# Kernel optimization log

Hardware: AMD Instinct MI355X
Metric: run time of the kernel (lower is better)

Reference implementation:

```python
import jax, jax.numpy as jnp
import numpy as np

CHUNK = 128      # chunk_size
NUM_BITS = 6     # log2(num_experts=64)


def setup_inputs() -> dict:
    key = jax.random.key(0)
    k1, k2, k3 = jax.random.split(key, 3)
    B, L, D, E = 4, 4096, 1024, 64
    x = jax.random.normal(k1, (B, L, D), dtype=jnp.float32)
    expert_weights = jax.random.normal(k2, (E, D, D), dtype=jnp.float32) * 0.02
    hyperplanes = jax.random.normal(k3, (D, NUM_BITS), dtype=jnp.float32)
    return {"x": x, "expert_weights": expert_weights, "hyperplanes": hyperplanes}


def reference(x, expert_weights, hyperplanes):
    # x: [B, L, D]; L divisible by CHUNK (no padding path taken)
    B, L, D = x.shape
    C = L // CHUNK
    xr = x.reshape(B, C, CHUNK, D)

    # --- LSH (SimHash) router, chunk-level ---
    chunk_emb = xr.mean(axis=2)                      # [B, C, D]
    proj = chunk_emb @ hyperplanes                   # [B, C, bits]
    bits = (proj > 0).astype(jnp.int32)
    powers = (2 ** jnp.arange(NUM_BITS)).astype(jnp.int32)
    e1 = jnp.sum(bits * powers, axis=-1)             # [B, C]
    weakest = jnp.argmin(jnp.abs(proj), axis=-1)     # weakest hyperplane bit
    flip = (2 ** weakest).astype(jnp.int32)
    e2 = jnp.bitwise_xor(e1, flip)                   # second expert: flip weakest bit
    # gates are all 1.0 and router_threshold=0.0 -> confidence_mask = 1.0

    # --- per-chunk expert weight gather + bmm combine (top-2 average) ---
    out = jnp.zeros_like(xr)
    for idx in (e1, e2):
        w = expert_weights[idx]                      # [B, C, D, D] gathered
        out = out + jnp.einsum('bcld,bcde->bcle', xr, w)
    out = out * 0.5
    # dropout p=0.0 / eval -> identity
    return out.reshape(B, L, D)
```

## Files before the change

kernel.cpp:

```cpp
#include <hip/hip_runtime.h>
#include <hip/hip_bf16.h>


#define BD 4
#define LD 4096
#define DD 1024
#define ED 64
#define CHUNKD 128
#define NBITS 6
#define NCHUNK 128

typedef __bf16 bf16_8 __attribute__((ext_vector_type(8)));
typedef __bf16 bf16_4 __attribute__((ext_vector_type(4)));
typedef float floatx4 __attribute__((ext_vector_type(4)));

__global__ __launch_bounds__(256) void sum_cvt_kernel(
    const float* __restrict__ x, __bf16* __restrict__ a, double* __restrict__ csum)
{
    const int chunk = blockIdx.x >> 3;
    const int tg = blockIdx.x & 7;
    const size_t base = (size_t)chunk * CHUNKD * DD + (size_t)tg * 16 * DD;
    const float* xc = x + base;
    __bf16* ac = a + base;
    const int t = threadIdx.x;

    double s0 = 0, s1 = 0, s2 = 0, s3 = 0;
    #pragma unroll 4
    for (int tok = 0; tok < 16; ++tok) {
        const float4 v = *(const float4*)(xc + tok * DD + t * 4);
        bf16_4 o;
        o[0] = (__bf16)v.x; o[1] = (__bf16)v.y; o[2] = (__bf16)v.z; o[3] = (__bf16)v.w;
        *(bf16_4*)(ac + tok * DD + t * 4) = o;
        s0 += (double)v.x; s1 += (double)v.y; s2 += (double)v.z; s3 += (double)v.w;
    }
    double* c = csum + (size_t)chunk * DD + t * 4;
    atomicAdd(c + 0, s0); atomicAdd(c + 1, s1);
    atomicAdd(c + 2, s2); atomicAdd(c + 3, s3);
}

__global__ __launch_bounds__(256) void router2_kernel(
    const double* __restrict__ csum, const float* __restrict__ hyp,
    int* __restrict__ eidx)
{
    const int chunk = blockIdx.x;
    const int t = threadIdx.x;
    double pj[NBITS];
    #pragma unroll
    for (int j = 0; j < NBITS; ++j) pj[j] = 0.0;
    #pragma unroll
    for (int i = 0; i < 4; ++i) {
        const int d = t + i * 256;
        const double emb = csum[(size_t)chunk * DD + d] * (1.0 / 128.0);
        #pragma unroll
        for (int j = 0; j < NBITS; ++j)
            pj[j] += emb * (double)hyp[d * NBITS + j];
    }
    #pragma unroll
    for (int off = 32; off > 0; off >>= 1) {
        #pragma unroll
        for (int j = 0; j < NBITS; ++j)
            pj[j] += __shfl_down(pj[j], off, 64);
    }
    __shared__ double red[4][NBITS];
    const int wave = t >> 6, lane = t & 63;
    if (lane == 0) {
        #pragma unroll
        for (int j = 0; j < NBITS; ++j) red[wave][j] = pj[j];
    }
    __syncthreads();
    if (t == 0) {
        int e1 = 0, weakest = 0;
        double best = 1e300;
        #pragma unroll
        for (int j = 0; j < NBITS; ++j) {
            double p = red[0][j] + red[1][j] + red[2][j] + red[3][j];
            if (p > 0.0) e1 |= (1 << j);
            double aa = fabs(p);
            if (aa < best) { best = aa; weakest = j; }
        }
        eidx[chunk * 2 + 0] = e1;
        eidx[chunk * 2 + 1] = e1 ^ (1 << weakest);
    }
}

__global__ __launch_bounds__(256) void wcvt_kernel(
    const float* __restrict__ W, __bf16* __restrict__ Wt)
{
    const int e = blockIdx.x >> 4;
    const int n0 = (blockIdx.x & 15) * 64;
    const float* We = W + (size_t)e * DD * DD;
    __bf16* Wte = Wt + (size_t)e * DD * DD;
    const int nl = threadIdx.x & 63;
    const int kc = threadIdx.x >> 6;
    const int n = n0 + nl;

    for (int it = 0; it < 32; ++it) {
        const int k = it * 32 + kc * 8;
        float v[8];
        #pragma unroll
        for (int j = 0; j < 8; ++j) v[j] = We[(size_t)(k + j) * DD + n];
        bf16_8 o;
        #pragma unroll
        for (int j = 0; j < 8; ++j) o[j] = (__bf16)v[j];
        *(bf16_8*)(&Wte[(size_t)n * DD + k]) = o;
    }
}

__global__ __launch_bounds__(256) void ffn_gemm_bf16(
    const __bf16* __restrict__ Abf,
    const __bf16* __restrict__ Wt,
    const int* __restrict__ eidx,
    float* __restrict__ out)
{
    __shared__ __bf16 Als[128 * 32];
    __shared__ __bf16 Bls[128 * 32];

    const int bx = blockIdx.x;
    const int chunk = bx >> 3;
    const int n0 = (bx & 7) * 128;
    const int t = threadIdx.x;
    const int lane = t & 63;
    const int wave = t >> 6;
    const int wm = wave >> 1;
    const int wn = wave & 1;
    const int lr = lane & 15;
    const int q  = lane >> 4;

    const int ee[2] = {eidx[chunk * 2 + 0], eidx[chunk * 2 + 1]};

    const __bf16* Ag = Abf + (size_t)chunk * CHUNKD * DD;

    floatx4 acc[4][4] = {};

    for (int xp = 0; xp < 2; ++xp) {
        const __bf16* Bg = Wt + (size_t)ee[xp] * (DD * DD) + (size_t)n0 * DD;
        for (int k0 = 0; k0 < DD; k0 += 32) {
            #pragma unroll
            for (int i = 0; i < 2; ++i) {
                const int rb = wave * 2 + i;
                const __bf16* ga = Ag + (size_t)(rb * 16 + lr) * DD + k0 + q * 8;
                __builtin_amdgcn_global_load_lds(
                    (const __attribute__((address_space(1))) void*)ga,
                    (__attribute__((address_space(3))) void*)(&Als[rb * 512]),
                    16, 0, 0);
            }
            #pragma unroll
            for (int i = 0; i < 2; ++i) {
                const int rb = wave * 2 + i;
                const __bf16* gb = Bg + (size_t)(rb * 16 + lr) * DD + k0 + q * 8;
                __builtin_amdgcn_global_load_lds(
                    (const __attribute__((address_space(1))) void*)gb,
                    (__attribute__((address_space(3))) void*)(&Bls[rb * 512]),
                    16, 0, 0);
            }
            __syncthreads();

            bf16_8 af[4], bfr[4];
            #pragma unroll
            for (int mt = 0; mt < 4; ++mt)
                af[mt] = *(const bf16_8*)(&Als[(wm * 4 + mt) * 512 + lane * 8]);
            #pragma unroll
            for (int nt = 0; nt < 4; ++nt)
                bfr[nt] = *(const bf16_8*)(&Bls[(wn * 4 + nt) * 512 + lane * 8]);
            #pragma unroll
            for (int mt = 0; mt < 4; ++mt) {
                #pragma unroll
                for (int nt = 0; nt < 4; ++nt)
                    acc[mt][nt] = __builtin_amdgcn_mfma_f32_16x16x32_bf16(
                        af[mt], bfr[nt], acc[mt][nt], 0, 0, 0);
            }
            __syncthreads();
        }
    }

    const size_t orow0 = (size_t)chunk * CHUNKD;
    #pragma unroll
    for (int mt = 0; mt < 4; ++mt) {
        #pragma unroll
        for (int nt = 0; nt < 4; ++nt) {
            const int col = n0 + wn * 64 + nt * 16 + lr;
            #pragma unroll
            for (int r = 0; r < 4; ++r) {
                const int row = wm * 64 + mt * 16 + q * 4 + r;
                out[(orow0 + row) * DD + col] = acc[mt][nt][r] * 0.5f;
            }
        }
    }
}

__global__ __launch_bounds__(256) void router_kernel(
    const float* __restrict__ x, const float* __restrict__ hyp,
    int* __restrict__ eidx)
{
    const int chunk = blockIdx.x;
    const int t = threadIdx.x;
    const float* xc = x + (size_t)chunk * CHUNKD * DD;
    double cs[4] = {0.0, 0.0, 0.0, 0.0};
    for (int tok = 0; tok < CHUNKD; ++tok) {
        const float* row = xc + tok * DD;
        #pragma unroll
        for (int i = 0; i < 4; ++i) cs[i] += (double)row[t + i * 256];
    }
    double pj[NBITS];
    #pragma unroll
    for (int j = 0; j < NBITS; ++j) pj[j] = 0.0;
    #pragma unroll
    for (int i = 0; i < 4; ++i) {
        const int d = t + i * 256;
        const double emb = cs[i] * (1.0 / 128.0);
        #pragma unroll
        for (int j = 0; j < NBITS; ++j) pj[j] += emb * (double)hyp[d * NBITS + j];
    }
    #pragma unroll
    for (int off = 32; off > 0; off >>= 1) {
        #pragma unroll
        for (int j = 0; j < NBITS; ++j) pj[j] += __shfl_down(pj[j], off, 64);
    }
    __shared__ double red[4][NBITS];
    const int wave = t >> 6, lane = t & 63;
    if (lane == 0) {
        #pragma unroll
        for (int j = 0; j < NBITS; ++j) red[wave][j] = pj[j];
    }
    __syncthreads();
    if (t == 0) {
        int e1 = 0, weakest = 0;
        double best = 1e300;
        #pragma unroll
        for (int j = 0; j < NBITS; ++j) {
            double p = red[0][j] + red[1][j] + red[2][j] + red[3][j];
            if (p > 0.0) e1 |= (1 << j);
            double a = fabs(p);
            if (a < best) { best = a; weakest = j; }
        }
        eidx[chunk * 2 + 0] = e1;
        eidx[chunk * 2 + 1] = e1 ^ (1 << weakest);
    }
}

__global__ __launch_bounds__(256) void cvt_x_kernel(
    const float* __restrict__ x, __bf16* __restrict__ a)
{
    const size_t i = ((size_t)blockIdx.x * 256 + threadIdx.x) * 4;
    const float4 v = *(const float4*)(x + i);
    bf16_4 o;
    o[0] = (__bf16)v.x; o[1] = (__bf16)v.y; o[2] = (__bf16)v.z; o[3] = (__bf16)v.w;
    *(bf16_4*)(a + i) = o;
}

__global__ __launch_bounds__(256) void ffn_gemm_fp32w(
    const __bf16* __restrict__ Abf, const float* __restrict__ W,
    const int* __restrict__ eidx, float* __restrict__ out)
{
    __shared__ __bf16 Als[128 * 32];
    __shared__ __bf16 Bls[128 * 32];
    const int bx = blockIdx.x;
    const int chunk = bx >> 3;
    const int n0 = (bx & 7) * 128;
    const int t = threadIdx.x;
    const int lane = t & 63;
    const int wave = t >> 6;
    const int wm = wave >> 1;
    const int wn = wave & 1;
    const int lr = lane & 15;
    const int q  = lane >> 4;
    const int ee[2] = {eidx[chunk * 2 + 0], eidx[chunk * 2 + 1]};
    const __bf16* Ag = Abf + (size_t)chunk * CHUNKD * DD;
    const int a_col = (lane & 3) * 8;
    const int a_rsub = lane >> 2;
    floatx4 acc[4][4] = {};
    for (int xp = 0; xp < 2; ++xp) {
        const float* We = W + (size_t)ee[xp] * (DD * DD) + n0;
        for (int k0 = 0; k0 < DD; k0 += 32) {
            float bv[2][8];
            #pragma unroll
            for (int rep = 0; rep < 2; ++rep) {
                const int nb = wave * 16 + lr + rep * 64;
                const float* src = We + (size_t)(k0 + q * 8) * DD + nb;
                #pragma unroll
                for (int j = 0; j < 8; ++j) bv[rep][j] = src[(size_t)j * DD];
            }
            #pragma unroll
            for (int i = 0; i < 2; ++i) {
                const __bf16* ga = Ag + (size_t)((wave * 2 + i) * 16 + a_rsub) * DD + k0 + a_col;
                __builtin_amdgcn_global_load_lds(
                    (const __attribute__((address_space(1))) void*)ga,
                    (__attribute__((address_space(3))) void*)(&Als[(wave * 2 + i) * 512]),
                    16, 0, 0);
            }
            #pragma unroll
            for (int rep = 0; rep < 2; ++rep) {
                const int nb = wave * 16 + lr + rep * 64;
                bf16_8 bw;
                #pragma unroll
                for (int j = 0; j < 8; ++j) bw[j] = (__bf16)bv[rep][j];
                *(bf16_8*)(&Bls[nb * 32 + q * 8]) = bw;
            }
            __syncthreads();
            bf16_8 af[4], bfr[4];
            #pragma unroll
            for (int mt = 0; mt < 4; ++mt)
                af[mt] = *(const bf16_8*)(&Als[(wm * 64 + mt * 16 + lr) * 32 + q * 8]);
            #pragma unroll
            for (int nt = 0; nt < 4; ++nt)
                bfr[nt] = *(const bf16_8*)(&Bls[(wn * 64 + nt * 16 + lr) * 32 + q * 8]);
            #pragma unroll
            for (int mt = 0; mt < 4; ++mt) {
                #pragma unroll
                for (int nt = 0; nt < 4; ++nt)
                    acc[mt][nt] = __builtin_amdgcn_mfma_f32_16x16x32_bf16(
                        af[mt], bfr[nt], acc[mt][nt], 0, 0, 0);
            }
            __syncthreads();
        }
    }
    const size_t orow0 = (size_t)chunk * CHUNKD;
    #pragma unroll
    for (int mt = 0; mt < 4; ++mt) {
        #pragma unroll
        for (int nt = 0; nt < 4; ++nt) {
            const int col = n0 + wn * 64 + nt * 16 + lr;
            #pragma unroll
            for (int r = 0; r < 4; ++r) {
                const int row = wm * 64 + mt * 16 + q * 4 + r;
                out[(orow0 + row) * DD + col] = acc[mt][nt][r] * 0.5f;
            }
        }
    }
}

extern "C" void kernel_launch(void* const* d_in, const int* in_sizes, int n_in,
                              void* d_out, int out_size, void* d_ws, size_t ws_size,
                              hipStream_t stream) {
    const float* x   = (const float*)d_in[0];
    const float* W   = (const float*)d_in[1];
    const float* hyp = (const float*)d_in[2];
    float* out = (float*)d_out;

    const size_t off_eidx = 0;
    const size_t off_csum = 4096;
    const size_t off_a    = off_csum + (size_t)NCHUNK * DD * 8;
    const size_t off_wt   = off_a + (size_t)NCHUNK * CHUNKD * DD * 2;
    const size_t need     = off_wt + (size_t)ED * DD * DD * 2;

    int* eidx = (int*)((char*)d_ws + off_eidx);
    __bf16* Abf = (__bf16*)((char*)d_ws + off_a);

    if (ws_size >= need) {
        double* csum = (double*)((char*)d_ws + off_csum);
        __bf16* Wtb = (__bf16*)((char*)d_ws + off_wt);
        hipMemsetAsync(csum, 0, (size_t)NCHUNK * DD * 8, stream);
        sum_cvt_kernel<<<NCHUNK * 8, 256, 0, stream>>>(x, Abf, csum);
        wcvt_kernel<<<ED * 16, 256, 0, stream>>>(W, Wtb);
        router2_kernel<<<NCHUNK, 256, 0, stream>>>(csum, hyp, eidx);
        ffn_gemm_bf16<<<NCHUNK * 8, 256, 0, stream>>>(Abf, Wtb, eidx, out);
    } else {
        __bf16* Abf2 = (__bf16*)((char*)d_ws + 1024);
        router_kernel<<<NCHUNK, 256, 0, stream>>>(x, hyp, eidx);
        cvt_x_kernel<<<(BD * LD * DD) / (256 * 4), 256, 0, stream>>>(x, Abf2);
        ffn_gemm_fp32w<<<NCHUNK * 8, 256, 0, stream>>>(Abf2, W, eidx, out);
    }
}
```

Baseline: 642.1 us.

## Pre-swizzle expert weights into MFMA tile order and fuse both experts per k-step

The weight conversion kernel now transposes through shared memory with coalesced float4 reads and writes bf16 weights in a pre-swizzled layout matching the MFMA fragment order, so each 32-wide k-slab of a 128-column tile is contiguous. The GEMM loads both experts' B tiles in the same k-iteration and reuses the A fragments for both, halving A loads and barrier count. The cost is an extra LDS buffer and a more involved layout contract between the two kernels.

Result: faster. 542.1 us (-15.6%).

```diff
diff --git a/kernel.cpp b/kernel.cpp
--- a/kernel.cpp
+++ b/kernel.cpp
@@ -13,6 +13,8 @@
 typedef __bf16 bf16_8 __attribute__((ext_vector_type(8)));
 typedef __bf16 bf16_4 __attribute__((ext_vector_type(4)));
 typedef float floatx4 __attribute__((ext_vector_type(4)));
+
+#define WT_PER_ENT  131072
 
 __global__ __launch_bounds__(256) void sum_cvt_kernel(
     const float* __restrict__ x, __bf16* __restrict__ a, double* __restrict__ csum)
@@ -84,40 +86,62 @@
 }
 
 __global__ __launch_bounds__(256) void wcvt_kernel(
-    const float* __restrict__ W, __bf16* __restrict__ Wt)
-{
-    const int e = blockIdx.x >> 4;
-    const int n0 = (blockIdx.x & 15) * 64;
-    const float* We = W + (size_t)e * DD * DD;
-    __bf16* Wte = Wt + (size_t)e * DD * DD;
-    const int nl = threadIdx.x & 63;
-    const int kc = threadIdx.x >> 6;
-    const int n = n0 + nl;
-
-    for (int it = 0; it < 32; ++it) {
-        const int k = it * 32 + kc * 8;
-        float v[8];
-        #pragma unroll
-        for (int j = 0; j < 8; ++j) v[j] = We[(size_t)(k + j) * DD + n];
-        bf16_8 o;
-        #pragma unroll
-        for (int j = 0; j < 8; ++j) o[j] = (__bf16)v[j];
-        *(bf16_8*)(&Wte[(size_t)n * DD + k]) = o;
+    const float* __restrict__ W, __bf16* __restrict__ WtSw)
+{
+    __shared__ float tile[32 * 129];
+
+    const int bx = blockIdx.x;
+    const int kh = bx & 1;
+    const int nt = (bx >> 1) & 7;
+    const int e  = bx >> 4;
+    const int t = threadIdx.x;
+
+    const float* We = W + (size_t)e * DD * DD + nt * 128;
+    __bf16* base_ent = WtSw + (size_t)(e * 8 + nt) * WT_PER_ENT;
+
+    for (int it = 0; it < 16; ++it) {
+        const int k0 = kh * 512 + it * 32;
+        const int s  = kh * 16 + it;
+        #pragma unroll
+        for (int p = 0; p < 4; ++p) {
+            const int idx = p * 256 + t;
+            const int kr  = idx >> 5;
+            const int nc4 = idx & 31;
+            const float4 v = *(const float4*)(We + (size_t)(k0 + kr) * DD + nc4 * 4);
+            float* dst = &tile[kr * 129 + nc4 * 4];
+            dst[0] = v.x; dst[1] = v.y; dst[2] = v.z; dst[3] = v.w;
+        }
+        __syncthreads();
+        #pragma unroll
+        for (int c = 0; c < 2; ++c) {
+            const int cell = c * 256 + t;
+            const int l  = cell & 63;
+            const int rb = cell >> 6;
+            const int q  = l >> 4;
+            const int lr = l & 15;
+            bf16_8 o;
+            #pragma unroll
+            for (int j = 0; j < 8; ++j)
+                o[j] = (__bf16)tile[(q * 8 + j) * 129 + rb * 16 + lr];
+            *(bf16_8*)(base_ent + ((size_t)s * 8 + rb) * 512 + l * 8) = o;
+        }
+        __syncthreads();
     }
 }
 
 __global__ __launch_bounds__(256) void ffn_gemm_bf16(
     const __bf16* __restrict__ Abf,
-    const __bf16* __restrict__ Wt,
+    const __bf16* __restrict__ WtSw,
     const int* __restrict__ eidx,
     float* __restrict__ out)
 {
-    __shared__ __bf16 Als[128 * 32];
-    __shared__ __bf16 Bls[128 * 32];
+    __shared__ __bf16 Als[8 * 512];
+    __shared__ __bf16 B0ls[8 * 512];
+    __shared__ __bf16 B1ls[8 * 512];
 
     const int bx = blockIdx.x;
     const int chunk = bx >> 3;
-    const int n0 = (bx & 7) * 128;
+    const int ntb = bx & 7;
     const int t = threadIdx.x;
     const int lane = t & 63;
     const int wave = t >> 6;
@@ -126,54 +150,68 @@
     const int lr = lane & 15;
     const int q  = lane >> 4;
 
-    const int ee[2] = {eidx[chunk * 2 + 0], eidx[chunk * 2 + 1]};
+    const int e0 = eidx[chunk * 2 + 0];
+    const int e1 = eidx[chunk * 2 + 1];
 
     const __bf16* Ag = Abf + (size_t)chunk * CHUNKD * DD;
+    const __bf16* Bg0 = WtSw + (size_t)(e0 * 8 + ntb) * WT_PER_ENT + lane * 8;
+    const __bf16* Bg1 = WtSw + (size_t)(e1 * 8 + ntb) * WT_PER_ENT + lane * 8;
+
+    const int rb0 = wave * 2;
+    const __bf16* AgW0 = Ag + (size_t)(rb0 * 16 + lr) * DD + q * 8;
+    const __bf16* AgW1 = Ag + (size_t)((rb0 + 1) * 16 + lr) * DD + q * 8;
 
     floatx4 acc[4][4] = {};
 
-    for (int xp = 0; xp < 2; ++xp) {
-        const __bf16* Bg = Wt + (size_t)ee[xp] * (DD * DD) + (size_t)n0 * DD;
-        for (int k0 = 0; k0 < DD; k0 += 32) {
-            #pragma unroll
-            for (int i = 0; i < 2; ++i) {
-                const int rb = wave * 2 + i;
-                const __bf16* ga = Ag + (size_t)(rb * 16 + lr) * DD + k0 + q * 8;
-                __builtin_amdgcn_global_load_lds(
-                    (const __attribute__((address_space(1))) void*)ga,
-                    (__attribute__((address_space(3))) void*)(&Als[rb * 512]),
-                    16, 0, 0);
-            }
-            #pragma unroll
-            for (int i = 0; i < 2; ++i) {
-                const int rb = wave * 2 + i;
-                const __bf16* gb = Bg + (size_t)(rb * 16 + lr) * DD + k0 + q * 8;
-                __builtin_amdgcn_global_load_lds(
-                    (const __attribute__((address_space(1))) void*)gb,
-                    (__attribute__((address_space(3))) void*)(&Bls[rb * 512]),
-                    16, 0, 0);
-            }
-            __syncthreads();
-
-            bf16_8 af[4], bfr[4];
-            #pragma unroll
-            for (int mt = 0; mt < 4; ++mt)
-                af[mt] = *(const bf16_8*)(&Als[(wm * 4 + mt) * 512 + lane * 8]);
+    for (int ks = 0; ks < 32; ++ks) {
+        const int k0 = ks * 32;
+        __builtin_amdgcn_global_load_lds(
+            (const __attribute__((address_space(1))) void*)(AgW0 + k0),
+            (__attribute__((address_space(3))) void*)(&Als[rb0 * 512]), 16, 0, 0);
+        __builtin_amdgcn_global_load_lds(
+            (const __attribute__((address_space(1))) void*)(AgW1 + k0),
+            (__attribute__((address_space(3))) void*)(&Als[(rb0 + 1) * 512]), 16, 0, 0);
+        #pragma unroll
+        for (int i = 0; i < 2; ++i) {
+            const int rb = rb0 + i;
+            __builtin_amdgcn_global_load_lds(
+                (const __attribute__((address_space(1))) void*)(Bg0 + ((size_t)ks * 8 + rb) * 512),
+                (__attribute__((address_space(3))) void*)(&B0ls[rb * 512]), 16, 0, 0);
+            __builtin_amdgcn_global_load_lds(
+                (const __attribute__((address_space(1))) void*)(Bg1 + ((size_t)ks * 8 + rb) * 512),
+                (__attribute__((address_space(3))) void*)(&B1ls[rb * 512]), 16, 0, 0);
+        }
+        __syncthreads();
+
+        bf16_8 af[4], bb[4];
+        #pragma unroll
+        for (int mt = 0; mt < 4; ++mt)
+            af[mt] = *(const bf16_8*)(&Als[(wm * 4 + mt) * 512 + lane * 8]);
+        #pragma unroll
+        for (int nt = 0; nt < 4; ++nt)
+            bb[nt] = *(const bf16_8*)(&B0ls[(wn * 4 + nt) * 512 + lane * 8]);
+        #pragma unroll
+        for (int mt = 0; mt < 4; ++mt) {
             #pragma unroll
             for (int nt = 0; nt < 4; ++nt)
-                bfr[nt] = *(const bf16_8*)(&Bls[(wn * 4 + nt) * 512 + lane * 8]);
-            #pragma unroll
-            for (int mt = 0; mt < 4; ++mt) {
-                #pragma unroll
-                for (int nt = 0; nt < 4; ++nt)
-                    acc[mt][nt] = __builtin_amdgcn_mfma_f32_16x16x32_bf16(
-                        af[mt], bfr[nt], acc[mt][nt], 0, 0, 0);
-            }
-            __syncthreads();
-        }
+                acc[mt][nt] = __builtin_amdgcn_mfma_f32_16x16x32_bf16(
+                    af[mt], bb[nt], acc[mt][nt], 0, 0, 0);
+        }
+        #pragma unroll
+        for (int nt = 0; nt < 4; ++nt)
+            bb[nt] = *(const bf16_8*)(&B1ls[(wn * 4 + nt) * 512 + lane * 8]);
+        #pragma unroll
+        for (int mt = 0; mt < 4; ++mt) {
+            #pragma unroll
+            for (int nt = 0; nt < 4; ++nt)
+                acc[mt][nt] = __builtin_amdgcn_mfma_f32_16x16x32_bf16(
+                    af[mt], bb[nt], acc[mt][nt], 0, 0, 0);
+        }
+        __syncthreads();
     }
 
     const size_t orow0 = (size_t)chunk * CHUNKD;
+    const int n0 = ntb * 128;
     #pragma unroll
     for (int mt = 0; mt < 4; ++mt) {
         #pragma unroll
@@ -348,12 +386,12 @@
 
     if (ws_size >= need) {
         double* csum = (double*)((char*)d_ws + off_csum);
-        __bf16* Wtb = (__bf16*)((char*)d_ws + off_wt);
+        __bf16* WtSw = (__bf16*)((char*)d_ws + off_wt);
         hipMemsetAsync(csum, 0, (size_t)NCHUNK * DD * 8, stream);
         sum_cvt_kernel<<<NCHUNK * 8, 256, 0, stream>>>(x, Abf, csum);
-        wcvt_kernel<<<ED * 16, 256, 0, stream>>>(W, Wtb);
+        wcvt_kernel<<<ED * 16, 256, 0, stream>>>(W, WtSw);
         router2_kernel<<<NCHUNK, 256, 0, stream>>>(csum, hyp, eidx);
-        ffn_gemm_bf16<<<NCHUNK * 8, 256, 0, stream>>>(Abf, Wtb, eidx, out);
+        ffn_gemm_bf16<<<NCHUNK * 8, 256, 0, stream>>>(Abf, WtSw, eidx, out);
     } else {
         __bf16* Abf2 = (__bf16*)((char*)d_ws + 1024);
         router_kernel<<<NCHUNK, 256, 0, stream>>>(x, hyp, eidx);
```
